# Performance work log

Hardware: AMD Instinct MI355X
Metric: run time of the kernel (lower is better)

Reference implementation:

```python
import jax, jax.numpy as jnp
import numpy as np

D_MODEL = 2048
HEADS = 16
HEAD_DIM = D_MODEL // HEADS
INNER = 8192
SEQ = 2048
EPS = 1e-5


def _layernorm(x, g, b):
    mu = jnp.mean(x, axis=-1, keepdims=True)
    var = jnp.mean(jnp.square(x - mu), axis=-1, keepdims=True)
    return (x - mu) * jax.lax.rsqrt(var + EPS) * g + b


def setup_inputs() -> dict:
    key = jax.random.key(0)
    ks = jax.random.split(key, 10)
    s = 0.02
    return {
        "x": jax.random.normal(ks[0], (1, SEQ, D_MODEL), dtype=jnp.float32),
        "C_w": jax.random.normal(ks[1], (D_MODEL, 3 * D_MODEL), dtype=jnp.float32) * s,
        "C_b": jnp.zeros((3 * D_MODEL,), dtype=jnp.float32),
        "lin_w": jax.random.normal(ks[2], (D_MODEL, D_MODEL), dtype=jnp.float32) * s,
        "lin_b": jnp.zeros((D_MODEL,), dtype=jnp.float32),
        "ff1_w": jax.random.normal(ks[3], (D_MODEL, INNER), dtype=jnp.float32) * s,
        "ff1_b": jnp.zeros((INNER,), dtype=jnp.float32),
        "ff2_w": jax.random.normal(ks[4], (INNER, D_MODEL), dtype=jnp.float32) * s,
        "ff2_b": jnp.zeros((D_MODEL,), dtype=jnp.float32),
        "ln1_g": jnp.ones((D_MODEL,), dtype=jnp.float32),
        "ln1_b": jnp.zeros((D_MODEL,), dtype=jnp.float32),
        "ln2_g": jnp.ones((D_MODEL,), dtype=jnp.float32),
        "ln2_b": jnp.zeros((D_MODEL,), dtype=jnp.float32),
    }


def reference(x, C_w, C_b, lin_w, lin_b, ff1_w, ff1_b, ff2_w, ff2_b,
              ln1_g, ln1_b, ln2_g, ln2_b):
    b, s, d = x.shape
    c = x @ C_w + C_b                       # [b, s, 3d]
    q, k, v = jnp.split(c, 3, axis=2)
    q = q.reshape(b, s, HEADS, HEAD_DIM)
    k = k.reshape(b, s, HEADS, HEAD_DIM)
    v = v.reshape(b, s, HEADS, HEAD_DIM)
    # NOTE: source scales by sqrt(d_model), NOT sqrt(head_dim)
    qk = jnp.einsum('bqhd,bkhd->bhqk', q, k) / jnp.sqrt(jnp.float32(d))
    causal = jnp.tril(jnp.ones((s, s), dtype=bool))  # [s, s]
    qk = jnp.where(causal[None, None, :, :], qk, -jnp.inf)
    scores = jax.nn.softmax(qk, axis=3)
    out = jnp.einsum('bhqk,bkhd->bqhd', scores, v).reshape(b, s, d)
    attn = out @ lin_w + lin_b
    h1 = _layernorm(x + attn, ln1_g, ln1_b)
    ff = jax.nn.gelu(h1 @ ff1_w + ff1_b, approximate=False) @ ff2_w + ff2_b
    return _layernorm(h1 + ff, ln2_g, ln2_b)
```

## Files before the change

### kernel.cpp

```cpp
#include <hip/hip_runtime.h>
#include <hip/hip_bf16.h>

#define SEQ 2048
#define DM 2048
#define NH 16
#define HD 128
#define FF 8192

typedef float f4v __attribute__((ext_vector_type(4)));
typedef short s8v __attribute__((ext_vector_type(8)));

__device__ __forceinline__ ushort f2bf(float f) {
  unsigned int x = __float_as_uint(f);
  unsigned int r = (x + 0x7FFFu + ((x >> 16) & 1u)) >> 16;
  return (ushort)r;
}

#define AS1 __attribute__((address_space(1)))
#define AS3 __attribute__((address_space(3)))
__device__ __forceinline__ void load16_lds(const ushort* g, ushort* l) {
  __builtin_amdgcn_global_load_lds((const AS1 unsigned int*)g, (AS3 unsigned int*)l, 16, 0, 0);
}

__global__ __launch_bounds__(256) void k_cvt(const float* __restrict__ in,
                                             ushort* __restrict__ out, int n4) {
  int i = blockIdx.x * 256 + threadIdx.x;
  if (i >= n4) return;
  f4v v = reinterpret_cast<const f4v*>(in)[i];
  ushort4 u;
  u.x = f2bf(v[0]); u.y = f2bf(v[1]); u.z = f2bf(v[2]); u.w = f2bf(v[3]);
  reinterpret_cast<ushort4*>(out)[i] = u;
}

__global__ __launch_bounds__(256) void k_tr(const float* __restrict__ W,
                                            ushort* __restrict__ Wt,
                                            int K, int N) {
  __shared__ float tile[32][36];
  int t = threadIdx.x;
  int n0 = blockIdx.x * 32, k0 = blockIdx.y * 32;
  int lr = t >> 3, lc = (t & 7) * 4;
  *(f4v*)&tile[lr][lc] = *(const f4v*)&W[(size_t)(k0 + lr) * N + n0 + lc];
  __syncthreads();
  int sn = t >> 3, sk = (t & 7) * 4;
  ushort4 u;
  u.x = f2bf(tile[sk + 0][sn]);
  u.y = f2bf(tile[sk + 1][sn]);
  u.z = f2bf(tile[sk + 2][sn]);
  u.w = f2bf(tile[sk + 3][sn]);
  *(ushort4*)&Wt[(size_t)(n0 + sn) * K + k0 + sk] = u;
}

__global__ __launch_bounds__(256) void k_gemm(const ushort* __restrict__ A,
                                              const ushort* __restrict__ Bt,
                                              const float* __restrict__ bias,
                                              float* __restrict__ Cf,
                                              ushort* __restrict__ Cb,
                                              int M, int N, int K, int gelu) {
  __shared__ ushort As[128 * 64];
  __shared__ ushort Bs[128 * 64];
  const int m0 = blockIdx.y * 128, n0 = blockIdx.x * 128;
  const int t = threadIdx.x;
  const int wave = t >> 6, lane = t & 63;
  const int wm = (wave >> 1) * 64, wn = (wave & 1) * 64;
  const int quad = lane >> 4, l16 = lane & 15;
  const int kchunk = K / gridDim.z;
  const int kbeg = blockIdx.z * kchunk, kend = kbeg + kchunk;
  if (Cf && gridDim.z > 1) Cf += (size_t)blockIdx.z * M * N;
  f4v acc[4][4] = {};
  const int srow = lane >> 3;
  const int scg = (lane & 7) ^ srow;
  const ushort* gA = A + (size_t)(m0 + wave * 32 + srow) * K + scg * 8;
  const ushort* gB = Bt + (size_t)(n0 + wave * 32 + srow) * K + scg * 8;
  ushort* lA = &As[(wave * 32) * 64];
  ushort* lB = &Bs[(wave * 32) * 64];

  for (int k0 = kbeg; k0 < kend; k0 += 64) {
#pragma unroll
    for (int p = 0; p < 4; ++p) {
      load16_lds(gA + (size_t)p * 8 * K + k0, lA + p * 8 * 64);
      load16_lds(gB + (size_t)p * 8 * K + k0, lB + p * 8 * 64);
    }
    __syncthreads();
#pragma unroll
    for (int kk = 0; kk < 64; kk += 32) {
      s8v af[4], bf[4];
#pragma unroll
      for (int i = 0; i < 4; ++i) {
        int ar = wm + i * 16 + l16;
        af[i] = *(const s8v*)&As[ar * 64 + ((((kk >> 3) + quad) ^ (ar & 7)) * 8)];
      }
#pragma unroll
      for (int j = 0; j < 4; ++j) {
        int br = wn + j * 16 + l16;
        bf[j] = *(const s8v*)&Bs[br * 64 + ((((kk >> 3) + quad) ^ (br & 7)) * 8)];
      }
#pragma unroll
      for (int i = 0; i < 4; ++i)
#pragma unroll
        for (int j = 0; j < 4; ++j)
          acc[i][j] = __builtin_amdgcn_mfma_f32_16x16x32_bf16(af[i], bf[j], acc[i][j], 0, 0, 0);
    }
    __syncthreads();
  }
#pragma unroll
  for (int i = 0; i < 4; ++i) {
    int rbase = m0 + wm + i * 16 + quad * 4;
#pragma unroll
    for (int j = 0; j < 4; ++j) {
      int cidx = n0 + wn + j * 16 + l16;
      float b = bias ? bias[cidx] : 0.0f;
#pragma unroll
      for (int r = 0; r < 4; ++r) {
        float v = acc[i][j][r] + b;
        if (gelu) v = 0.5f * v * (1.0f + erff(v * 0.70710678118654752f));
        if (Cf) Cf[(size_t)(rbase + r) * N + cidx] = v;
        if (Cb) Cb[(size_t)(rbase + r) * N + cidx] = f2bf(v);
      }
    }
  }
}

__global__ __launch_bounds__(256) void k_attn_mfma(const ushort* __restrict__ qkv,
                                                   ushort* __restrict__ ctx) {
  __shared__ ushort Ks[64][136];
  __shared__ ushort Vt[128][72];
  __shared__ ushort Ps[4][16][72];
  const int idx = blockIdx.x;
  const int h = idx & (NH - 1);
  const int qt = (SEQ / 64 - 1) - (idx >> 4);
  const int q0 = qt * 64;
  const int t = threadIdx.x;
  const int wave = t >> 6, lane = t & 63;
  const int quad = lane >> 4, l16 = lane & 15;
  const float scale = 0.022097086912079608f;

  s8v aq[4];
  {
    const ushort* qp = qkv + (size_t)(q0 + 16 * wave + l16) * (3 * DM) + h * HD + quad * 8;
#pragma unroll
    for (int ks = 0; ks < 4; ++ks)
      aq[ks] = *(const s8v*)(qp + ks * 32);
  }
  f4v acc_o[8] = {};
  float m_r[4], l_r[4];
#pragma unroll
  for (int r = 0; r < 4; ++r) { m_r[r] = -1e30f; l_r[r] = 0.0f; }

  for (int kt = 0; kt <= qt; ++kt) {
    const int k0 = kt * 64;
    __syncthreads();
    {
      const ushort* kp = qkv + (size_t)k0 * (3 * DM) + DM + h * HD;
#pragma unroll
      for (int i = 0; i < 4; ++i) {
        int ch = t + i * 256;
        int row = ch >> 4, c8 = (ch & 15) * 8;
        *(s8v*)&Ks[row][c8] = *(const s8v*)(kp + (size_t)row * (3 * DM) + c8);
      }
      const ushort* vp = qkv + (size_t)k0 * (3 * DM) + 2 * DM + h * HD;
#pragma unroll
      for (int i = 0; i < 4; ++i) {
        int id = t + i * 256;
        int d = id & 127, sg = id >> 7;
        ushort e0 = vp[(size_t)(sg * 8 + 0) * (3 * DM) + d];
        ushort e1 = vp[(size_t)(sg * 8 + 1) * (3 * DM) + d];
        ushort e2 = vp[(size_t)(sg * 8 + 2) * (3 * DM) + d];
        ushort e3 = vp[(size_t)(sg * 8 + 3) * (3 * DM) + d];
        ushort e4 = vp[(size_t)(sg * 8 + 4) * (3 * DM) + d];
        ushort e5 = vp[(size_t)(sg * 8 + 5) * (3 * DM) + d];
        ushort e6 = vp[(size_t)(sg * 8 + 6) * (3 * DM) + d];
        ushort e7 = vp[(size_t)(sg * 8 + 7) * (3 * DM) + d];
        uint4 pk;
        pk.x = (uint)e0 | ((uint)e1 << 16);
        pk.y = (uint)e2 | ((uint)e3 << 16);
        pk.z = (uint)e4 | ((uint)e5 << 16);
        pk.w = (uint)e6 | ((uint)e7 << 16);
        *(uint4*)&Vt[d][sg * 8] = pk;
      }
    }
    __syncthreads();

    f4v sacc[4] = {};
#pragma unroll
    for (int ks = 0; ks < 4; ++ks) {
      s8v bk[4];
#pragma unroll
      for (int j = 0; j < 4; ++j)
        bk[j] = *(const s8v*)&Ks[j * 16 + l16][ks * 32 + quad * 8];
#pragma unroll
      for (int j = 0; j < 4; ++j)
        sacc[j] = __builtin_amdgcn_mfma_f32_16x16x32_bf16(aq[ks], bk[j], sacc[j], 0, 0, 0);
    }
    if (kt == qt) {
#pragma unroll
      for (int j = 0; j < 4; ++j)
#pragma unroll
        for (int r = 0; r < 4; ++r) {
          int lrow = 16 * wave + quad * 4 + r;
          int lcol = j * 16 + l16;
          sacc[j][r] = (lcol > lrow) ? -1e30f : sacc[j][r] * scale;
        }
    } else {
#pragma unroll
      for (int j = 0; j < 4; ++j)
#pragma unroll
        for (int r = 0; r < 4; ++r) sacc[j][r] *= scale;
    }
    float alpha[4];
#pragma unroll
    for (int r = 0; r < 4; ++r) {
      float mx = fmaxf(fmaxf(sacc[0][r], sacc[1][r]), fmaxf(sacc[2][r], sacc[3][r]));
      mx = fmaxf(mx, __shfl_xor(mx, 1));
      mx = fmaxf(mx, __shfl_xor(mx, 2));
      mx = fmaxf(mx, __shfl_xor(mx, 4));
      mx = fmaxf(mx, __shfl_xor(mx, 8));
      float mn = fmaxf(m_r[r], mx);
      alpha[r] = __expf(m_r[r] - mn);
      m_r[r] = mn;
      float ps = 0.0f;
#pragma unroll
      for (int j = 0; j < 4; ++j) {
        float p = __expf(sacc[j][r] - mn);
        sacc[j][r] = p;
        ps += p;
      }
      ps += __shfl_xor(ps, 1);
      ps += __shfl_xor(ps, 2);
      ps += __shfl_xor(ps, 4);
      ps += __shfl_xor(ps, 8);
      l_r[r] = l_r[r] * alpha[r] + ps;
    }
#pragma unroll
    for (int j = 0; j < 4; ++j)
#pragma unroll
      for (int r = 0; r < 4; ++r)
        Ps[wave][quad * 4 + r][j * 16 + l16] = f2bf(sacc[j][r]);
#pragma unroll
    for (int nd = 0; nd < 8; ++nd)
#pragma unroll
      for (int r = 0; r < 4; ++r) acc_o[nd][r] *= alpha[r];
#pragma unroll
    for (int ks2 = 0; ks2 < 2; ++ks2) {
      s8v ap = *(const s8v*)&Ps[wave][l16][ks2 * 32 + quad * 8];
#pragma unroll
      for (int nd = 0; nd < 8; ++nd) {
        s8v bv = *(const s8v*)&Vt[nd * 16 + l16][ks2 * 32 + quad * 8];
        acc_o[nd] = __builtin_amdgcn_mfma_f32_16x16x32_bf16(ap, bv, acc_o[nd], 0, 0, 0);
      }
    }
  }
  float rl[4];
#pragma unroll
  for (int r = 0; r < 4; ++r) rl[r] = 1.0f / l_r[r];
#pragma unroll
  for (int nd = 0; nd < 8; ++nd) {
    int col = h * HD + nd * 16 + l16;
#pragma unroll
    for (int r = 0; r < 4; ++r) {
      int row = q0 + 16 * wave + quad * 4 + r;
      ctx[(size_t)row * DM + col] = f2bf(acc_o[nd][r] * rl[r]);
    }
  }
}

__global__ __launch_bounds__(256) void k_ln_sk(const float* __restrict__ A,
                                               const float* __restrict__ P, int np,
                                               const float* __restrict__ bias,
                                               const float* __restrict__ g,
                                               const float* __restrict__ be,
                                               float* __restrict__ outf,
                                               ushort* __restrict__ outb) {
  int row = blockIdx.x;
  int t = threadIdx.x;
  const f4v* av = reinterpret_cast<const f4v*>(A + (size_t)row * DM);
  f4v x0 = av[t];
  f4v x1 = av[t + 256];
  for (int s = 0; s < np; ++s) {
    const f4v* pv = reinterpret_cast<const f4v*>(P + (size_t)s * SEQ * DM + (size_t)row * DM);
    x0 += pv[t];
    x1 += pv[t + 256];
  }
  const f4v* bb = reinterpret_cast<const f4v*>(bias);
  x0 += bb[t];
  x1 += bb[t + 256];
  float s = x0[0] + x0[1] + x0[2] + x0[3] + x1[0] + x1[1] + x1[2] + x1[3];
  float q = x0[0]*x0[0] + x0[1]*x0[1] + x0[2]*x0[2] + x0[3]*x0[3]
          + x1[0]*x1[0] + x1[1]*x1[1] + x1[2]*x1[2] + x1[3]*x1[3];
#pragma unroll
  for (int off = 32; off; off >>= 1) {
    s += __shfl_down(s, off, 64);
    q += __shfl_down(q, off, 64);
  }
  __shared__ float rs[4], rq[4];
  if ((t & 63) == 0) { rs[t >> 6] = s; rq[t >> 6] = q; }
  __syncthreads();
  s = rs[0] + rs[1] + rs[2] + rs[3];
  q = rq[0] + rq[1] + rq[2] + rq[3];
  float mu = s * (1.0f / DM);
  float var = q * (1.0f / DM) - mu * mu;
  float rstd = rsqrtf(var + 1e-5f);
  const f4v* gv = reinterpret_cast<const f4v*>(g);
  const f4v* bev = reinterpret_cast<const f4v*>(be);
  f4v y0 = (x0 - mu) * rstd * gv[t] + bev[t];
  f4v y1 = (x1 - mu) * rstd * gv[t + 256] + bev[t + 256];
  reinterpret_cast<f4v*>(outf + (size_t)row * DM)[t] = y0;
  reinterpret_cast<f4v*>(outf + (size_t)row * DM)[t + 256] = y1;
  if (outb) {
    ushort4 u0, u1;
    u0.x = f2bf(y0[0]); u0.y = f2bf(y0[1]); u0.z = f2bf(y0[2]); u0.w = f2bf(y0[3]);
    u1.x = f2bf(y1[0]); u1.y = f2bf(y1[1]); u1.z = f2bf(y1[2]); u1.w = f2bf(y1[3]);
    reinterpret_cast<ushort4*>(outb + (size_t)row * DM)[t] = u0;
    reinterpret_cast<ushort4*>(outb + (size_t)row * DM)[t + 256] = u1;
  }
}

extern "C" void kernel_launch(void* const* d_in, const int* in_sizes, int n_in,
                              void* d_out, int out_size, void* d_ws, size_t ws_size,
                              hipStream_t stream) {
  const float* x     = (const float*)d_in[0];
  const float* C_w   = (const float*)d_in[1];
  const float* C_b   = (const float*)d_in[2];
  const float* lin_w = (const float*)d_in[3];
  const float* lin_b = (const float*)d_in[4];
  const float* ff1_w = (const float*)d_in[5];
  const float* ff1_b = (const float*)d_in[6];
  const float* ff2_w = (const float*)d_in[7];
  const float* ff2_b = (const float*)d_in[8];
  const float* ln1g  = (const float*)d_in[9];
  const float* ln1b  = (const float*)d_in[10];
  const float* ln2g  = (const float*)d_in[11];
  const float* ln2b  = (const float*)d_in[12];

  char* ws = (char*)d_ws;
  size_t off = 0;
  auto take = [&](size_t bytes) {
    char* p = ws + off;
    off += (bytes + 255) & ~(size_t)255;
    return p;
  };
  ushort* Wt   = (ushort*)take((size_t)FF * DM * 2);
  ushort* qkvb = (ushort*)take((size_t)SEQ * 3 * DM * 2);
  ushort* xb   = (ushort*)take((size_t)SEQ * DM * 2);
  ushort* ctxb = (ushort*)take((size_t)SEQ * DM * 2);
  ushort* bigb = (ushort*)take((size_t)SEQ * FF * 2);
  float*  h1   = (float*) take((size_t)SEQ * DM * 4);
  float*  part = (float*) take((size_t)4 * SEQ * DM * 4);

  k_cvt<<<SEQ * DM / 1024, 256, 0, stream>>>(x, xb, SEQ * DM / 4);
  k_tr<<<dim3(3 * DM / 32, DM / 32), 256, 0, stream>>>(C_w, Wt, DM, 3 * DM);
  k_gemm<<<dim3(3 * DM / 128, SEQ / 128, 1), 256, 0, stream>>>(xb, Wt, C_b, nullptr, qkvb, SEQ, 3 * DM, DM, 0);
  k_attn_mfma<<<dim3((SEQ / 64) * NH), 256, 0, stream>>>(qkvb, ctxb);
  k_tr<<<dim3(DM / 32, DM / 32), 256, 0, stream>>>(lin_w, Wt, DM, DM);
  k_gemm<<<dim3(DM / 128, SEQ / 128, 4), 256, 0, stream>>>(ctxb, Wt, nullptr, part, nullptr, SEQ, DM, DM, 0);
  k_ln_sk<<<SEQ, 256, 0, stream>>>(x, part, 4, lin_b, ln1g, ln1b, h1, xb);
  k_tr<<<dim3(FF / 32, DM / 32), 256, 0, stream>>>(ff1_w, Wt, DM, FF);
  k_gemm<<<dim3(FF / 128, SEQ / 128, 1), 256, 0, stream>>>(xb, Wt, ff1_b, nullptr, bigb, SEQ, FF, DM, 1);
  k_tr<<<dim3(DM / 32, FF / 32), 256, 0, stream>>>(ff2_w, Wt, FF, DM);
  k_gemm<<<dim3(DM / 128, SEQ / 128, 4), 256, 0, stream>>>(bigb, Wt, nullptr, part, nullptr, SEQ, DM, FF, 0);
  k_ln_sk<<<SEQ, 256, 0, stream>>>(h1, part, 4, ff2_b, ln2g, ln2b, (float*)d_out, (ushort*)nullptr);
}
```

Measured before the change: 651.8 us.

## Load GEMM B operand directly to registers, bf16 split-K partials, tanh GELU

The GEMM stops staging the B tile in LDS and has each wave load its B fragments straight from global memory, halving LDS use and adding an occupancy hint of 4 blocks per CU. Split-K partial sums are written as bf16 instead of fp32, which halves the partial-buffer traffic read by the layernorm kernels. The exact erf GELU is replaced with a tanh/exp approximation to cut epilogue cost. These trade coalesced, LDS-shared B loads for uncached per-lane global reads, and they add rounding error from the bf16 partials and the approximate GELU.

Result: slower. 784.5 us (+20.4%).

```diff
diff --git a/kernel.cpp b/kernel.cpp
--- a/kernel.cpp
+++ b/kernel.cpp
@@ -14,6 +14,13 @@
   unsigned int x = __float_as_uint(f);
   unsigned int r = (x + 0x7FFFu + ((x >> 16) & 1u)) >> 16;
   return (ushort)r;
+}
+__device__ __forceinline__ float bf2f(ushort u) {
+  return __uint_as_float((unsigned int)u << 16);
+}
+__device__ __forceinline__ float gelu_f(float v) {
+  float u = 0.7978845608028654f * v * (1.0f + 0.044715f * v * v);
+  return v / (1.0f + __expf(-2.0f * u));
 }
 
 #define AS1 __attribute__((address_space(1)))
@@ -50,51 +57,52 @@
   *(ushort4*)&Wt[(size_t)(n0 + sn) * K + k0 + sk] = u;
 }
 
-__global__ __launch_bounds__(256) void k_gemm(const ushort* __restrict__ A,
-                                              const ushort* __restrict__ Bt,
-                                              const float* __restrict__ bias,
-                                              float* __restrict__ Cf,
-                                              ushort* __restrict__ Cb,
-                                              int M, int N, int K, int gelu) {
+__global__ __launch_bounds__(256, 4) void k_gemm(const ushort* __restrict__ A,
+                                                 const ushort* __restrict__ Bt,
+                                                 const float* __restrict__ bias,
+                                                 float* __restrict__ Cf,
+                                                 ushort* __restrict__ Cb,
+                                                 int M, int N, int K, int gelu) {
   __shared__ ushort As[128 * 64];
-  __shared__ ushort Bs[128 * 64];
   const int m0 = blockIdx.y * 128, n0 = blockIdx.x * 128;
   const int t = threadIdx.x;
   const int wave = t >> 6, lane = t & 63;
   const int wm = (wave >> 1) * 64, wn = (wave & 1) * 64;
   const int quad = lane >> 4, l16 = lane & 15;
   const int kchunk = K / gridDim.z;
-  const int kbeg = blockIdx.z * kchunk, kend = kbeg + kchunk;
-  if (Cf && gridDim.z > 1) Cf += (size_t)blockIdx.z * M * N;
+  const int kbeg = blockIdx.z * kchunk;
+  if (gridDim.z > 1) {
+    if (Cf) Cf += (size_t)blockIdx.z * M * N;
+    if (Cb) Cb += (size_t)blockIdx.z * M * N;
+  }
   f4v acc[4][4] = {};
   const int srow = lane >> 3;
   const int scg = (lane & 7) ^ srow;
-  const ushort* gA = A + (size_t)(m0 + wave * 32 + srow) * K + scg * 8;
-  const ushort* gB = Bt + (size_t)(n0 + wave * 32 + srow) * K + scg * 8;
+  const ushort* gA = A + (size_t)(m0 + wave * 32 + srow) * K + scg * 8 + kbeg;
   ushort* lA = &As[(wave * 32) * 64];
-  ushort* lB = &Bs[(wave * 32) * 64];
-
-  for (int k0 = kbeg; k0 < kend; k0 += 64) {
-#pragma unroll
-    for (int p = 0; p < 4; ++p) {
-      load16_lds(gA + (size_t)p * 8 * K + k0, lA + p * 8 * 64);
-      load16_lds(gB + (size_t)p * 8 * K + k0, lB + p * 8 * 64);
-    }
+  const ushort* pB0 = Bt + (size_t)(n0 + wn + 0 * 16 + l16) * K + quad * 8 + kbeg;
+  const ushort* pB1 = Bt + (size_t)(n0 + wn + 1 * 16 + l16) * K + quad * 8 + kbeg;
+  const ushort* pB2 = Bt + (size_t)(n0 + wn + 2 * 16 + l16) * K + quad * 8 + kbeg;
+  const ushort* pB3 = Bt + (size_t)(n0 + wn + 3 * 16 + l16) * K + quad * 8 + kbeg;
+
+  for (int kof = 0; kof < kchunk; kof += 64) {
+#pragma unroll
+    for (int p = 0; p < 4; ++p)
+      load16_lds(gA + (size_t)p * 8 * K + kof, lA + p * 8 * 64);
     __syncthreads();
 #pragma unroll
     for (int kk = 0; kk < 64; kk += 32) {
       s8v af[4], bf[4];
+      bf[0] = *(const s8v*)(pB0 + kof + kk);
+      bf[1] = *(const s8v*)(pB1 + kof + kk);
+      bf[2] = *(const s8v*)(pB2 + kof + kk);
+      bf[3] = *(const s8v*)(pB3 + kof + kk);
 #pragma unroll
       for (int i = 0; i < 4; ++i) {
         int ar = wm + i * 16 + l16;
         af[i] = *(const s8v*)&As[ar * 64 + ((((kk >> 3) + quad) ^ (ar & 7)) * 8)];
       }
 #pragma unroll
-      for (int j = 0; j < 4; ++j) {
-        int br = wn + j * 16 + l16;
-        bf[j] = *(const s8v*)&Bs[br * 64 + ((((kk >> 3) + quad) ^ (br & 7)) * 8)];
-      }
-#pragma unroll
       for (int i = 0; i < 4; ++i)
 #pragma unroll
         for (int j = 0; j < 4; ++j)
@@ -112,7 +120,7 @@
 #pragma unroll
       for (int r = 0; r < 4; ++r) {
         float v = acc[i][j][r] + b;
-        if (gelu) v = 0.5f * v * (1.0f + erff(v * 0.70710678118654752f));
+        if (gelu) v = gelu_f(v);
         if (Cf) Cf[(size_t)(rbase + r) * N + cidx] = v;
         if (Cb) Cb[(size_t)(rbase + r) * N + cidx] = f2bf(v);
       }
@@ -264,7 +272,7 @@
 }
 
 __global__ __launch_bounds__(256) void k_ln_sk(const float* __restrict__ A,
-                                               const float* __restrict__ P, int np,
+                                               const ushort* __restrict__ P, int np,
                                                const float* __restrict__ bias,
                                                const float* __restrict__ g,
                                                const float* __restrict__ be,
@@ -276,9 +284,10 @@
   f4v x0 = av[t];
   f4v x1 = av[t + 256];
   for (int s = 0; s < np; ++s) {
-    const f4v* pv = reinterpret_cast<const f4v*>(P + (size_t)s * SEQ * DM + (size_t)row * DM);
-    x0 += pv[t];
-    x1 += pv[t + 256];
+    const ushort4* pv = reinterpret_cast<const ushort4*>(P + (size_t)s * SEQ * DM + (size_t)row * DM);
+    ushort4 p0 = pv[t], p1 = pv[t + 256];
+    x0[0] += bf2f(p0.x); x0[1] += bf2f(p0.y); x0[2] += bf2f(p0.z); x0[3] += bf2f(p0.w);
+    x1[0] += bf2f(p1.x); x1[1] += bf2f(p1.y); x1[2] += bf2f(p1.z); x1[3] += bf2f(p1.w);
   }
   const f4v* bb = reinterpret_cast<const f4v*>(bias);
   x0 += bb[t];
@@ -344,18 +353,18 @@
   ushort* ctxb = (ushort*)take((size_t)SEQ * DM * 2);
   ushort* bigb = (ushort*)take((size_t)SEQ * FF * 2);
   float*  h1   = (float*) take((size_t)SEQ * DM * 4);
-  float*  part = (float*) take((size_t)4 * SEQ * DM * 4);
+  ushort* part = (ushort*)take((size_t)4 * SEQ * DM * 2);
 
   k_cvt<<<SEQ * DM / 1024, 256, 0, stream>>>(x, xb, SEQ * DM / 4);
   k_tr<<<dim3(3 * DM / 32, DM / 32), 256, 0, stream>>>(C_w, Wt, DM, 3 * DM);
   k_gemm<<<dim3(3 * DM / 128, SEQ / 128, 1), 256, 0, stream>>>(xb, Wt, C_b, nullptr, qkvb, SEQ, 3 * DM, DM, 0);
   k_attn_mfma<<<dim3((SEQ / 64) * NH), 256, 0, stream>>>(qkvb, ctxb);
   k_tr<<<dim3(DM / 32, DM / 32), 256, 0, stream>>>(lin_w, Wt, DM, DM);
-  k_gemm<<<dim3(DM / 128, SEQ / 128, 4), 256, 0, stream>>>(ctxb, Wt, nullptr, part, nullptr, SEQ, DM, DM, 0);
+  k_gemm<<<dim3(DM / 128, SEQ / 128, 4), 256, 0, stream>>>(ctxb, Wt, nullptr, nullptr, part, SEQ, DM, DM, 0);
   k_ln_sk<<<SEQ, 256, 0, stream>>>(x, part, 4, lin_b, ln1g, ln1b, h1, xb);
   k_tr<<<dim3(FF / 32, DM / 32), 256, 0, stream>>>(ff1_w, Wt, DM, FF);
   k_gemm<<<dim3(FF / 128, SEQ / 128, 1), 256, 0, stream>>>(xb, Wt, ff1_b, nullptr, bigb, SEQ, FF, DM, 1);
   k_tr<<<dim3(DM / 32, FF / 32), 256, 0, stream>>>(ff2_w, Wt, FF, DM);
-  k_gemm<<<dim3(DM / 128, SEQ / 128, 4), 256, 0, stream>>>(bigb, Wt, nullptr, part, nullptr, SEQ, DM, FF, 0);
+  k_gemm<<<dim3(DM / 128, SEQ / 128, 4), 256, 0, stream>>>(bigb, Wt, nullptr, nullptr, part, SEQ, DM, FF, 0);
   k_ln_sk<<<SEQ, 256, 0, stream>>>(h1, part, 4, ff2_b, ln2g, ln2b, (float*)d_out, (ushort*)nullptr);
 }
```
